# Kernel optimization log

Measured on AMD Instinct MI355X. Metric: run time of the kernel, lower is better.

## Reference

```python
import math
import jax, jax.numpy as jnp
import numpy as np

B, T, QDIM, ADIM = 256, 2048, 1024, 128
DC, DK = 8, 21          # dynamic channels / kernel
SC, SK = 8, 21          # static channels / kernel
PL, ALPHA, BETA = 11, 0.1, 0.9


def _betabinom_pmf_flipped(n, a, b, length):
    lg = np.vectorize(math.lgamma)
    k = np.arange(length, dtype=np.float64)
    logp = (lg(n + 1.0) - lg(k + 1.0) - lg(n - k + 1.0)
            + lg(k + a) + lg(n - k + b) - lg(n + a + b)
            - (lg(a) + lg(b) - lg(a + b)))
    return np.exp(logp)[::-1].copy()  # .flip(0) as in the torch buffer


def setup_inputs() -> dict:
    key = jax.random.key(0)
    ks = jax.random.split(key, 10)

    def lin(k, shape, fan_in):
        return (jax.random.normal(k, shape, jnp.float32) / np.sqrt(fan_in)).astype(jnp.float32)

    query = jax.random.normal(ks[0], (B, QDIM), jnp.float32)
    # previous-step alignment: a valid probability distribution over T
    alignment_pre = jax.nn.softmax(2.0 * jax.random.normal(ks[1], (B, T), jnp.float32), axis=1)

    P = jnp.asarray(_betabinom_pmf_flipped(PL - 1, ALPHA, BETA, PL), jnp.float32)
    W_w = lin(ks[2], (ADIM, QDIM), QDIM)
    W_b = jnp.zeros((ADIM,), jnp.float32)
    V_w = lin(ks[3], (DC * DK, ADIM), ADIM)
    F_w = lin(ks[4], (SC, 1, SK), SK)        # Conv1d(1, SC, SK) weight
    U_w = lin(ks[5], (ADIM, SC), SC)
    T_w = lin(ks[6], (ADIM, DC), DC)
    T_b = jnp.zeros((ADIM,), jnp.float32)
    v_w = lin(ks[7], (1, ADIM), ADIM)
    return {"query": query, "alignment_pre": alignment_pre, "P": P,
            "W_w": W_w, "W_b": W_b, "V_w": V_w, "F_w": F_w,
            "U_w": U_w, "T_w": T_w, "T_b": T_b, "v_w": v_w}


def reference(query, alignment_pre, P, W_w, W_b, V_w, F_w, U_w, T_w, T_b, v_w):
    b, t = alignment_pre.shape
    pad = (DK - 1) // 2  # == PL - 1 == 10, shared by all three convs
    x_pad = jnp.pad(alignment_pre, ((0, 0), (pad, pad)))
    # sliding windows (cross-correlation layout): windows[b, t, k] = x_pad[b, t + k]
    windows = jnp.stack([x_pad[:, k:k + t] for k in range(DK)], axis=-1)  # (B, T, DK)

    # prior: causal conv with left pad PL-1 == windows taps 0..PL-1
    p = jnp.log(jnp.clip(jnp.einsum('btk,k->bt', windows[..., :PL], P), 1e-6))

    # per-sample dynamic kernels
    G = jnp.tanh(query @ W_w.T + W_b) @ V_w.T          # (B, DC*DK)
    G = G.reshape(b, DC, DK)
    g = jnp.einsum('btk,bck->btc', windows, G)          # grouped conv, groups=B -> (B, T, DC)

    # static conv over previous alignment
    f = jnp.einsum('btk,ck->btc', windows, F_w[:, 0, :])  # (B, T, SC)

    e = jnp.squeeze(jnp.tanh(f @ U_w.T + g @ T_w.T + T_b) @ v_w.T, -1) + p  # (B, T)
    return jax.nn.softmax(e, axis=1)
```

## Files before the change

### kernel.cpp

```cpp
#include <hip/hip_runtime.h>
#include <hip/hip_bf16.h>

#define Bsz 256
#define Tn 2048
#define QD 1024
#define AD 128
#define DCn 8
#define DKn 21
#define PLn 11
#define GN (DCn * DKn)
#define XS2 24

typedef _Float16 f16x8 __attribute__((ext_vector_type(8)));
typedef float f32x4 __attribute__((ext_vector_type(4)));

#define TWO_LOG2E 2.8853900817779268f

__global__ __launch_bounds__(512) void g_kernel(
    const float* __restrict__ query, const float* __restrict__ W_w,
    const float* __restrict__ W_b, const float* __restrict__ V_w,
    float* __restrict__ G_ws)
{
    __shared__ float h_lds[AD];
    const int b    = blockIdx.x;
    const int tid  = threadIdx.x;
    const int w    = tid >> 6;
    const int lane = tid & 63;

    const float4* q4 = (const float4*)(query + b * QD);
    float4 q0 = q4[lane];
    float4 q1 = q4[64 + lane];
    float4 q2 = q4[128 + lane];
    float4 q3 = q4[192 + lane];

    #pragma unroll 2
    for (int i = 0; i < 16; ++i) {
        int a = w * 16 + i;
        const float4* w4 = (const float4*)(W_w + a * QD);
        float4 x0 = w4[lane];
        float4 x1 = w4[64 + lane];
        float4 x2 = w4[128 + lane];
        float4 x3 = w4[192 + lane];
        float accA = 0.f, accB = 0.f;
        accA = fmaf(q0.x, x0.x, fmaf(q0.y, x0.y, fmaf(q0.z, x0.z, fmaf(q0.w, x0.w, accA))));
        accB = fmaf(q1.x, x1.x, fmaf(q1.y, x1.y, fmaf(q1.z, x1.z, fmaf(q1.w, x1.w, accB))));
        accA = fmaf(q2.x, x2.x, fmaf(q2.y, x2.y, fmaf(q2.z, x2.z, fmaf(q2.w, x2.w, accA))));
        accB = fmaf(q3.x, x3.x, fmaf(q3.y, x3.y, fmaf(q3.z, x3.z, fmaf(q3.w, x3.w, accB))));
        float acc = accA + accB;
        #pragma unroll
        for (int off = 32; off; off >>= 1) acc += __shfl_xor(acc, off);
        if (lane == 0) h_lds[a] = tanhf(acc + W_b[a]);
    }
    __syncthreads();

    for (int r = w; r < GN; r += 8) {
        float acc = fmaf(h_lds[lane], V_w[r * AD + lane],
                         h_lds[64 + lane] * V_w[r * AD + 64 + lane]);
        #pragma unroll
        for (int off = 32; off; off >>= 1) acc += __shfl_xor(acc, off);
        if (lane == 0) G_ws[b * GN + r] = acc;
    }
}

__global__ __launch_bounds__(1024, 4) void e_kernel(
    const float* __restrict__ align, const float* __restrict__ P,
    const float* __restrict__ F_w, const float* __restrict__ U_w,
    const float* __restrict__ T_w, const float* __restrict__ T_b,
    const float* __restrict__ v_w, const float* __restrict__ G_ws,
    float* __restrict__ out)
{
    __shared__ float    al32[Tn + 20];
    __shared__ _Float16 al16[Tn + 44];
    __shared__ float    pcb[Tn];
    __shared__ float    sden[Tn];
    __shared__ _Float16 Xw[16 * 2 * 16 * XS2];
    __shared__ float    red[16];
    __shared__ float    bc;

    const int b    = blockIdx.x;
    const int tid  = threadIdx.x;
    const int lane = tid & 63;
    const int wid  = tid >> 6;
    const int l15  = lane & 15;
    const int quad = lane >> 4;

    for (int i = tid; i < Tn + 44; i += 1024) {
        int s = i - 10;
        float v = (s >= 0 && s < Tn) ? align[b * Tn + s] : 0.f;
        if (i < Tn + 20) al32[i] = v;
        al16[i] = (_Float16)v;
    }

    f16x8 Bc = {};
    #pragma unroll
    for (int j = 0; j < 8; ++j) {
        int k = quad * 8 + j;
        float wv = 0.f;
        if (k < DKn) wv = (l15 < 8) ? F_w[l15 * DKn + k]
                                    : G_ws[b * GN + (l15 - 8) * DKn + k];
        Bc[j] = (_Float16)wv;
    }

    f16x8 Bf[8];
    float vn2[8], tb2[8];
    float vsum = 0.f;
    #pragma unroll
    for (int n = 0; n < 8; ++n) {
        int a = n * 16 + l15;
        f16x8 bf = {};
        const float* src = (quad == 0) ? (U_w + a * 8) : (T_w + a * 8);
        if (quad < 2) {
            float4 lo = ((const float4*)src)[0];
            float4 hi = ((const float4*)src)[1];
            bf[0] = (_Float16)(TWO_LOG2E * lo.x); bf[1] = (_Float16)(TWO_LOG2E * lo.y);
            bf[2] = (_Float16)(TWO_LOG2E * lo.z); bf[3] = (_Float16)(TWO_LOG2E * lo.w);
            bf[4] = (_Float16)(TWO_LOG2E * hi.x); bf[5] = (_Float16)(TWO_LOG2E * hi.y);
            bf[6] = (_Float16)(TWO_LOG2E * hi.z); bf[7] = (_Float16)(TWO_LOG2E * hi.w);
        }
        Bf[n] = bf;
        float va = v_w[a];
        vn2[n] = -2.f * va;
        vsum  += va;
        tb2[n] = TWO_LOG2E * T_b[a];
    }
    #pragma unroll
    for (int off = 1; off <= 8; off <<= 1) vsum += __shfl_xor(vsum, off);
    __syncthreads();

    #pragma unroll
    for (int tt = 0; tt < 2; ++tt) {
        int t = tid + tt * 1024;
        float pr = 0.f;
        #pragma unroll
        for (int k = 0; k < PLn; ++k) pr = fmaf(al32[t + k], P[k], pr);
        pcb[t] = fmaxf(pr, 1e-6f);
    }
    __syncthreads();

    const int t0w = wid * 128;
    _Float16* Xp0 = &Xw[wid * 2 * 16 * XS2];
    _Float16* Xp1 = Xp0 + 16 * XS2;
    float wsum = 0.f;

    #pragma unroll 1
    for (int m = 0; m < 8; m += 2) {
        const int ta = t0w + m * 16;
        const int tb_ = ta + 16;

        f16x8 Ac0, Ac1;
        #pragma unroll
        for (int j = 0; j < 8; ++j) {
            Ac0[j] = al16[ta  + l15 + quad * 8 + j];
            Ac1[j] = al16[tb_ + l15 + quad * 8 + j];
        }
        f32x4 z = {};
        f32x4 X0 = __builtin_amdgcn_mfma_f32_16x16x32_f16(Ac0, Bc, z, 0, 0, 0);
        f32x4 X1 = __builtin_amdgcn_mfma_f32_16x16x32_f16(Ac1, Bc, z, 0, 0, 0);

        #pragma unroll
        for (int r = 0; r < 4; ++r) {
            Xp0[(quad * 4 + r) * XS2 + l15] = (_Float16)X0[r];
            Xp1[(quad * 4 + r) * XS2 + l15] = (_Float16)X1[r];
        }
        __asm__ __volatile__("" ::: "memory");

        f16x8 A20 = {}, A21 = {};
        if (quad < 2) {
            A20 = *(const f16x8*)&Xp0[l15 * XS2 + quad * 8];
            A21 = *(const f16x8*)&Xp1[l15 * XS2 + quad * 8];
        }

        float esA[4] = {0.f, 0.f, 0.f, 0.f};
        float esB[4] = {0.f, 0.f, 0.f, 0.f};
        #pragma unroll
        for (int n = 0; n < 8; ++n) {
            f32x4 z2 = {};
            f32x4 d0 = __builtin_amdgcn_mfma_f32_16x16x32_f16(A20, Bf[n], z2, 0, 0, 0);
            f32x4 d1 = __builtin_amdgcn_mfma_f32_16x16x32_f16(A21, Bf[n], z2, 0, 0, 0);
            #pragma unroll
            for (int r = 0; r < 4; ++r) {
                float qa = __builtin_amdgcn_exp2f(d0[r] + tb2[n]);
                float qb = __builtin_amdgcn_exp2f(d1[r] + tb2[n]);
                float ra = __builtin_amdgcn_rcpf(qa + 1.f);
                float rb = __builtin_amdgcn_rcpf(qb + 1.f);
                esA[r] = fmaf(vn2[n], ra, esA[r]);
                esB[r] = fmaf(vn2[n], rb, esB[r]);
            }
        }
        #pragma unroll
        for (int off = 1; off <= 8; off <<= 1) {
            #pragma unroll
            for (int r = 0; r < 4; ++r) {
                esA[r] += __shfl_xor(esA[r], off);
                esB[r] += __shfl_xor(esB[r], off);
            }
        }
        if (l15 < 4) {
            float evA = ((l15 == 0) ? esA[0] : (l15 == 1) ? esA[1]
                       : (l15 == 2) ? esA[2] : esA[3]) + vsum;
            float evB = ((l15 == 0) ? esB[0] : (l15 == 1) ? esB[1]
                       : (l15 == 2) ? esB[2] : esB[3]) + vsum;
            int tA = ta  + quad * 4 + l15;
            int tB = tb_ + quad * 4 + l15;
            float svA = pcb[tA] * __expf(evA);
            float svB = pcb[tB] * __expf(evB);
            sden[tA] = svA;
            sden[tB] = svB;
            wsum += svA + svB;
        }
    }

    __syncthreads();
    #pragma unroll
    for (int off = 32; off; off >>= 1) wsum += __shfl_xor(wsum, off);
    if (lane == 0) red[wid] = wsum;
    __syncthreads();
    if (wid == 0) {
        float ss = (lane < 16) ? red[lane] : 0.f;
        #pragma unroll
        for (int off = 8; off; off >>= 1) ss += __shfl_xor(ss, off);
        if (lane == 0) bc = ss;
    }
    __syncthreads();
    const float inv = 1.f / bc;
    out[b * Tn + tid]        = sden[tid] * inv;
    out[b * Tn + tid + 1024] = sden[tid + 1024] * inv;
}

extern "C" void kernel_launch(void* const* d_in, const int* in_sizes, int n_in,
                              void* d_out, int out_size, void* d_ws, size_t ws_size,
                              hipStream_t stream) {
    const float* query = (const float*)d_in[0];
    const float* align = (const float*)d_in[1];
    const float* P     = (const float*)d_in[2];
    const float* W_w   = (const float*)d_in[3];
    const float* W_b   = (const float*)d_in[4];
    const float* V_w   = (const float*)d_in[5];
    const float* F_w   = (const float*)d_in[6];
    const float* U_w   = (const float*)d_in[7];
    const float* T_w   = (const float*)d_in[8];
    const float* T_b   = (const float*)d_in[9];
    const float* v_w   = (const float*)d_in[10];
    float* out  = (float*)d_out;
    float* G_ws = (float*)d_ws;

    g_kernel<<<Bsz, 512, 0, stream>>>(query, W_w, W_b, V_w, G_ws);
    e_kernel<<<Bsz, 1024, 0, stream>>>(align, P, F_w, U_w, T_w, T_b, v_w, G_ws, out);
}
```

Baseline: 120.1 us.

## Fuse dynamic-kernel computation into attention kernel and transpose second MFMA

Merges the per-sample G computation (query projection, tanh, V projection) into the main energy kernel, so G stays in LDS and one launch plus the global workspace round trip go away. The second MFMA swaps its operands so each lane's outputs lie along the attention dimension. The bias is folded into the MFMA through a constant-one K slot, which replaces the 16-lane shuffle reduction with two shuffles. The prior conv now reads the fp16 alignment copy, dropping the fp32 LDS buffer at some precision cost, and every block redoes the W_w matvec serially before the main work starts.

```diff
diff --git a/kernel.cpp b/kernel.cpp
--- a/kernel.cpp
+++ b/kernel.cpp
@@ -16,64 +16,20 @@
 
 #define TWO_LOG2E 2.8853900817779268f
 
-__global__ __launch_bounds__(512) void g_kernel(
-    const float* __restrict__ query, const float* __restrict__ W_w,
+__global__ __launch_bounds__(1024, 4) void dca_kernel(
+    const float* __restrict__ query, const float* __restrict__ align,
+    const float* __restrict__ P, const float* __restrict__ W_w,
     const float* __restrict__ W_b, const float* __restrict__ V_w,
-    float* __restrict__ G_ws)
-{
-    __shared__ float h_lds[AD];
-    const int b    = blockIdx.x;
-    const int tid  = threadIdx.x;
-    const int w    = tid >> 6;
-    const int lane = tid & 63;
-
-    const float4* q4 = (const float4*)(query + b * QD);
-    float4 q0 = q4[lane];
-    float4 q1 = q4[64 + lane];
-    float4 q2 = q4[128 + lane];
-    float4 q3 = q4[192 + lane];
-
-    #pragma unroll 2
-    for (int i = 0; i < 16; ++i) {
-        int a = w * 16 + i;
-        const float4* w4 = (const float4*)(W_w + a * QD);
-        float4 x0 = w4[lane];
-        float4 x1 = w4[64 + lane];
-        float4 x2 = w4[128 + lane];
-        float4 x3 = w4[192 + lane];
-        float accA = 0.f, accB = 0.f;
-        accA = fmaf(q0.x, x0.x, fmaf(q0.y, x0.y, fmaf(q0.z, x0.z, fmaf(q0.w, x0.w, accA))));
-        accB = fmaf(q1.x, x1.x, fmaf(q1.y, x1.y, fmaf(q1.z, x1.z, fmaf(q1.w, x1.w, accB))));
-        accA = fmaf(q2.x, x2.x, fmaf(q2.y, x2.y, fmaf(q2.z, x2.z, fmaf(q2.w, x2.w, accA))));
-        accB = fmaf(q3.x, x3.x, fmaf(q3.y, x3.y, fmaf(q3.z, x3.z, fmaf(q3.w, x3.w, accB))));
-        float acc = accA + accB;
-        #pragma unroll
-        for (int off = 32; off; off >>= 1) acc += __shfl_xor(acc, off);
-        if (lane == 0) h_lds[a] = tanhf(acc + W_b[a]);
-    }
-    __syncthreads();
-
-    for (int r = w; r < GN; r += 8) {
-        float acc = fmaf(h_lds[lane], V_w[r * AD + lane],
-                         h_lds[64 + lane] * V_w[r * AD + 64 + lane]);
-        #pragma unroll
-        for (int off = 32; off; off >>= 1) acc += __shfl_xor(acc, off);
-        if (lane == 0) G_ws[b * GN + r] = acc;
-    }
-}
-
-__global__ __launch_bounds__(1024, 4) void e_kernel(
-    const float* __restrict__ align, const float* __restrict__ P,
     const float* __restrict__ F_w, const float* __restrict__ U_w,
     const float* __restrict__ T_w, const float* __restrict__ T_b,
-    const float* __restrict__ v_w, const float* __restrict__ G_ws,
-    float* __restrict__ out)
+    const float* __restrict__ v_w, float* __restrict__ out)
 {
-    __shared__ float    al32[Tn + 20];
     __shared__ _Float16 al16[Tn + 44];
     __shared__ float    pcb[Tn];
     __shared__ float    sden[Tn];
     __shared__ _Float16 Xw[16 * 2 * 16 * XS2];
+    __shared__ float    h_lds[AD];
+    __shared__ float    G_lds[GN];
     __shared__ float    red[16];
     __shared__ float    bc;
 
@@ -87,9 +43,53 @@
     for (int i = tid; i < Tn + 44; i += 1024) {
         int s = i - 10;
         float v = (s >= 0 && s < Tn) ? align[b * Tn + s] : 0.f;
-        if (i < Tn + 20) al32[i] = v;
         al16[i] = (_Float16)v;
     }
+
+    {
+        const float4* q4 = (const float4*)(query + b * QD);
+        float4 q0 = q4[lane];
+        float4 q1 = q4[64 + lane];
+        float4 q2 = q4[128 + lane];
+        float4 q3 = q4[192 + lane];
+        #pragma unroll 2
+        for (int i = 0; i < 8; ++i) {
+            int a = wid * 8 + i;
+            const float4* w4 = (const float4*)(W_w + a * QD);
+            float4 x0 = w4[lane];
+            float4 x1 = w4[64 + lane];
+            float4 x2 = w4[128 + lane];
+            float4 x3 = w4[192 + lane];
+            float accA = 0.f, accB = 0.f;
+            accA = fmaf(q0.x, x0.x, fmaf(q0.y, x0.y, fmaf(q0.z, x0.z, fmaf(q0.w, x0.w, accA))));
+            accB = fmaf(q1.x, x1.x, fmaf(q1.y, x1.y, fmaf(q1.z, x1.z, fmaf(q1.w, x1.w, accB))));
+            accA = fmaf(q2.x, x2.x, fmaf(q2.y, x2.y, fmaf(q2.z, x2.z, fmaf(q2.w, x2.w, accA))));
+            accB = fmaf(q3.x, x3.x, fmaf(q3.y, x3.y, fmaf(q3.z, x3.z, fmaf(q3.w, x3.w, accB))));
+            float acc = accA + accB;
+            #pragma unroll
+            for (int off = 32; off; off >>= 1) acc += __shfl_xor(acc, off);
+            if (lane == 0) h_lds[a] = tanhf(acc + W_b[a]);
+        }
+    }
+    __syncthreads();
+
+    if (tid < GN) {
+        float g = 0.f;
+        #pragma unroll 4
+        for (int i = 0; i < AD; ++i) g = fmaf(h_lds[i], V_w[tid * AD + i], g);
+        G_lds[tid] = g;
+    }
+
+    const int t0w = wid * 128;
+    #pragma unroll
+    for (int tt = 0; tt < 2; ++tt) {
+        int t = t0w + tt * 64 + lane;
+        float pr = 0.f;
+        #pragma unroll
+        for (int k = 0; k < PLn; ++k) pr = fmaf((float)al16[t + k], P[k], pr);
+        pcb[t] = fmaxf(pr, 1e-6f);
+    }
+    __syncthreads();
 
     f16x8 Bc = {};
     #pragma unroll
@@ -97,54 +97,48 @@
         int k = quad * 8 + j;
         float wv = 0.f;
         if (k < DKn) wv = (l15 < 8) ? F_w[l15 * DKn + k]
-                                    : G_ws[b * GN + (l15 - 8) * DKn + k];
+                                    : G_lds[(l15 - 8) * DKn + k];
         Bc[j] = (_Float16)wv;
     }
 
     f16x8 Bf[8];
-    float vn2[8], tb2[8];
-    float vsum = 0.f;
     #pragma unroll
     for (int n = 0; n < 8; ++n) {
         int a = n * 16 + l15;
         f16x8 bf = {};
-        const float* src = (quad == 0) ? (U_w + a * 8) : (T_w + a * 8);
         if (quad < 2) {
+            const float* src = (quad == 0) ? (U_w + a * 8) : (T_w + a * 8);
             float4 lo = ((const float4*)src)[0];
             float4 hi = ((const float4*)src)[1];
             bf[0] = (_Float16)(TWO_LOG2E * lo.x); bf[1] = (_Float16)(TWO_LOG2E * lo.y);
             bf[2] = (_Float16)(TWO_LOG2E * lo.z); bf[3] = (_Float16)(TWO_LOG2E * lo.w);
             bf[4] = (_Float16)(TWO_LOG2E * hi.x); bf[5] = (_Float16)(TWO_LOG2E * hi.y);
             bf[6] = (_Float16)(TWO_LOG2E * hi.z); bf[7] = (_Float16)(TWO_LOG2E * hi.w);
+        } else if (quad == 2) {
+            bf[0] = (_Float16)(TWO_LOG2E * T_b[a]);
         }
         Bf[n] = bf;
-        float va = v_w[a];
-        vn2[n] = -2.f * va;
-        vsum  += va;
-        tb2[n] = TWO_LOG2E * T_b[a];
-    }
-    #pragma unroll
-    for (int off = 1; off <= 8; off <<= 1) vsum += __shfl_xor(vsum, off);
-    __syncthreads();
-
-    #pragma unroll
-    for (int tt = 0; tt < 2; ++tt) {
-        int t = tid + tt * 1024;
-        float pr = 0.f;
-        #pragma unroll
-        for (int k = 0; k < PLn; ++k) pr = fmaf(al32[t + k], P[k], pr);
-        pcb[t] = fmaxf(pr, 1e-6f);
-    }
-    __syncthreads();
-
-    const int t0w = wid * 128;
+    }
+
+    f32x4 vnq[8];
+    float vsum = 0.f;
+    #pragma unroll
+    for (int n = 0; n < 8; ++n) {
+        f32x4 vq = *(const f32x4*)(v_w + n * 16 + quad * 4);
+        vsum += vq[0] + vq[1] + vq[2] + vq[3];
+        vq[0] *= -2.f; vq[1] *= -2.f; vq[2] *= -2.f; vq[3] *= -2.f;
+        vnq[n] = vq;
+    }
+    vsum += __shfl_xor(vsum, 16);
+    vsum += __shfl_xor(vsum, 32);
+
     _Float16* Xp0 = &Xw[wid * 2 * 16 * XS2];
     _Float16* Xp1 = Xp0 + 16 * XS2;
     float wsum = 0.f;
 
     #pragma unroll 1
     for (int m = 0; m < 8; m += 2) {
-        const int ta = t0w + m * 16;
+        const int ta  = t0w + m * 16;
         const int tb_ = ta + 16;
 
         f16x8 Ac0, Ac1;
@@ -164,46 +158,41 @@
         }
         __asm__ __volatile__("" ::: "memory");
 
-        f16x8 A20 = {}, A21 = {};
+        f16x8 B20 = {}, B21 = {};
         if (quad < 2) {
-            A20 = *(const f16x8*)&Xp0[l15 * XS2 + quad * 8];
-            A21 = *(const f16x8*)&Xp1[l15 * XS2 + quad * 8];
-        }
-
-        float esA[4] = {0.f, 0.f, 0.f, 0.f};
-        float esB[4] = {0.f, 0.f, 0.f, 0.f};
+            B20 = *(const f16x8*)&Xp0[l15 * XS2 + quad * 8];
+            B21 = *(const f16x8*)&Xp1[l15 * XS2 + quad * 8];
+        } else if (quad == 2) {
+            B20[0] = (_Float16)1.f;
+            B21[0] = (_Float16)1.f;
+        }
+
+        float es0 = 0.f, es1 = 0.f;
         #pragma unroll
         for (int n = 0; n < 8; ++n) {
             f32x4 z2 = {};
-            f32x4 d0 = __builtin_amdgcn_mfma_f32_16x16x32_f16(A20, Bf[n], z2, 0, 0, 0);
-            f32x4 d1 = __builtin_amdgcn_mfma_f32_16x16x32_f16(A21, Bf[n], z2, 0, 0, 0);
+            f32x4 d0 = __builtin_amdgcn_mfma_f32_16x16x32_f16(Bf[n], B20, z2, 0, 0, 0);
+            f32x4 d1 = __builtin_amdgcn_mfma_f32_16x16x32_f16(Bf[n], B21, z2, 0, 0, 0);
             #pragma unroll
             for (int r = 0; r < 4; ++r) {
-                float qa = __builtin_amdgcn_exp2f(d0[r] + tb2[n]);
-                float qb = __builtin_amdgcn_exp2f(d1[r] + tb2[n]);
+                float qa = __builtin_amdgcn_exp2f(d0[r]);
+                float qb = __builtin_amdgcn_exp2f(d1[r]);
                 float ra = __builtin_amdgcn_rcpf(qa + 1.f);
                 float rb = __builtin_amdgcn_rcpf(qb + 1.f);
-                esA[r] = fmaf(vn2[n], ra, esA[r]);
-                esB[r] = fmaf(vn2[n], rb, esB[r]);
+                es0 = fmaf(vnq[n][r], ra, es0);
+                es1 = fmaf(vnq[n][r], rb, es1);
             }
         }
-        #pragma unroll
-        for (int off = 1; off <= 8; off <<= 1) {
-            #pragma unroll
-            for (int r = 0; r < 4; ++r) {
-                esA[r] += __shfl_xor(esA[r], off);
-                esB[r] += __shfl_xor(esB[r], off);
-            }
-        }
-        if (l15 < 4) {
-            float evA = ((l15 == 0) ? esA[0] : (l15 == 1) ? esA[1]
-                       : (l15 == 2) ? esA[2] : esA[3]) + vsum;
-            float evB = ((l15 == 0) ? esB[0] : (l15 == 1) ? esB[1]
-                       : (l15 == 2) ? esB[2] : esB[3]) + vsum;
-            int tA = ta  + quad * 4 + l15;
-            int tB = tb_ + quad * 4 + l15;
-            float svA = pcb[tA] * __expf(evA);
-            float svB = pcb[tB] * __expf(evB);
+        es0 += __shfl_xor(es0, 16);
+        es0 += __shfl_xor(es0, 32);
+        es1 += __shfl_xor(es1, 16);
+        es1 += __shfl_xor(es1, 32);
+
+        if (lane < 16) {
+            int tA = ta  + lane;
+            int tB = tb_ + lane;
+            float svA = pcb[tA] * __expf(es0 + vsum);
+            float svB = pcb[tB] * __expf(es1 + vsum);
             sden[tA] = svA;
             sden[tB] = svB;
             wsum += svA + svB;
@@ -241,9 +230,8 @@
     const float* T_w   = (const float*)d_in[8];
     const float* T_b   = (const float*)d_in[9];
     const float* v_w   = (const float*)d_in[10];
-    float* out  = (float*)d_out;
-    float* G_ws = (float*)d_ws;
-
-    g_kernel<<<Bsz, 512, 0, stream>>>(query, W_w, W_b, V_w, G_ws);
-    e_kernel<<<Bsz, 1024, 0, stream>>>(align, P, F_w, U_w, T_w, T_b, v_w, G_ws, out);
+    float* out = (float*)d_out;
+
+    dca_kernel<<<Bsz, 1024, 0, stream>>>(query, align, P, W_w, W_b, V_w,
+                                         F_w, U_w, T_w, T_b, v_w, out);
 }
```

After: 106.0 us. 1.13x faster.
